# Kernel tuning notes

Hardware: AMD Instinct MI355X
Metric: run time of the kernel (lower is better)

The kernel has to match this reference:

```python
import jax, jax.numpy as jnp
import numpy as np

MAX_SHIFT = 20
DAILY_CYCLE = 288
HORIZON_OFFSET = 1


def _valid_shifts(T):
    shifts = sorted(set(list(range(-MAX_SHIFT, 1)) + [-(DAILY_CYCLE - HORIZON_OFFSET)]))
    return [s for s in shifts if 0 < abs(s) < T]


def setup_inputs() -> dict:
    key = jax.random.key(0)
    k1, k2 = jax.random.split(key)
    x = jax.random.normal(k1, (2, 320, 207, 64), dtype=jnp.float32)
    w = jax.random.normal(k2, (1, 1), dtype=jnp.float32)  # LearnableSimilarity linear weight
    return {"x": x, "w": w}


def reference(x, w):
    B, T, L, D = x.shape
    shifts = _valid_shifts(T)
    S = len(shifts)  # 21 for T=320

    # Build zero-padded shifted copies: for s<0, shifted[:, t] = x[:, t+|s|] (zeros at tail).
    sh_list = []
    for s in shifts:
        p = abs(s)
        pad = jnp.zeros((B, p, L, D), dtype=x.dtype)
        if s < 0:
            sh_list.append(jnp.concatenate([x[:, p:], pad], axis=1))
        else:
            sh_list.append(jnp.concatenate([pad, x[:, :-p]], axis=1))
    xs = jnp.stack(sh_list, axis=1)  # [B, S, T, L, D]

    # Learnable similarity = (x . y) * w; mean over T fused into the einsum.
    wscalar = w[0, 0]
    sim_avg = jnp.einsum('btld,bstmd->bslm', x, xs) * (wscalar / T)  # [B,S,L,L]  l=target, m=shifted

    # Faithful to original: softmax over joint (S*target-L) axis, then raw reshape to (L, S*L).
    flat = sim_avg.reshape(B, S * L, L)
    soft = jax.nn.softmax(flat, axis=1)
    attn = soft.reshape(B, L, S * L)  # NOTE: reshape, not transpose (matches torch .view)

    x_flat = xs.transpose(0, 2, 1, 3, 4).reshape(B, T, S * L, D)  # m index = s*L + link
    out = jnp.einsum('btmd,blm->btld', x_flat, attn)  # [B,T,L,D]
    return out
```

## Files before the change

kernel.cpp:

```cpp
#include <hip/hip_runtime.h>
#include <hip/hip_bf16.h>

#define B_DIM 2
#define T_DIM 320
#define L_DIM 207
#define D_DIM 64
#define S_DIM 21
#define J_TOT (S_DIM * L_DIM)
#define MPAD 224
#define IPAD 256
#define NSPLIT 4
#define TSPLIT 80
#define NCH_A 32
#define CH_A 136
#define NCH_P 128
#define CH_P 34
#define LD_ROW (L_DIM * D_DIM)

typedef __attribute__((ext_vector_type(8))) short bf16x8;
typedef __attribute__((ext_vector_type(4))) float f32x4;

__device__ inline unsigned short f2bf(float f) {
    unsigned int u = __builtin_bit_cast(unsigned int, f);
    u = (u + 0x7FFFu + ((u >> 16) & 1u)) >> 16;
    return (unsigned short)u;
}

__device__ inline int shift_p(int s) { return (s == 0) ? 287 : (21 - s); }
__device__ inline int imin(int a, int b) { return a < b ? a : b; }
__device__ inline int imax(int a, int b) { return a > b ? a : b; }

__device__ __forceinline__ void glds16(const void* g, void* l) {
    __builtin_amdgcn_global_load_lds(
        (const __attribute__((address_space(1))) void*)g,
        (__attribute__((address_space(3))) void*)l,
        16, 0, 0);
}

__global__ void __launch_bounds__(256) k_prep(const float* __restrict__ x,
                                              unsigned short* __restrict__ xbf,
                                              unsigned short* __restrict__ xt) {
    __shared__ float tile[L_DIM * 66];
    int bt = blockIdx.x;
    const float* src = x + (size_t)bt * LD_ROW;
    int tid = threadIdx.x;
    for (int idx = tid; idx < L_DIM * D_DIM; idx += 256) {
        int l = idx >> 6, d = idx & 63;
        tile[l * 66 + d] = src[idx];
    }
    __syncthreads();
    unsigned short* dst1 = xbf + (size_t)bt * LD_ROW;
    for (int idx = tid; idx < L_DIM * D_DIM; idx += 256) {
        int l = idx >> 6, d = idx & 63;
        dst1[idx] = f2bf(tile[l * 66 + d]);
    }
    unsigned short* dst2 = xt + (size_t)bt * (7 * 64 * 32);
    if (tid < MPAD) {
        int mc = tid >> 5, mi = tid & 31;
        for (int d = 0; d < D_DIM; ++d) {
            float v = (tid < L_DIM) ? tile[tid * 66 + d] : 0.0f;
            dst2[(mc * 64 + d) * 32 + mi] = f2bf(v);
        }
    }
}

__global__ void __launch_bounds__(256) k_sim(const unsigned short* __restrict__ xbf,
                                             float* __restrict__ part) {
    __shared__ __align__(16) unsigned short S[2][2][8192];

    int id = blockIdx.x;
    int bsplit = id & 7;
    int b = bsplit >> 2, split = bsplit & 3;
    int rest = id >> 3;
    int s = rest >> 2;
    int tile = rest & 3;
    int l0 = (tile >> 1) * 128, m0 = (tile & 1) * 128;

    int p = shift_p(s);
    int nt = T_DIM - p;
    int t0 = (split * nt) >> 2;
    int t1 = (((split + 1) * nt) >> 2);

    int tid = threadIdx.x;
    int wave = tid >> 6, lane = tid & 63;
    int wl = wave >> 1, wm = wave & 1;
    int fr = lane & 15, kg = lane >> 4;
    int x7 = fr & 7;

    int rN = 0, cN = 0;
#pragma unroll
    for (int g = 0; g < 4; ++g) {
        if (l0 + (g * 2 + wl) * 16 < L_DIM) rN = g + 1;
        if (m0 + (g * 2 + wm) * 16 < L_DIM) cN = g + 1;
    }

    int srcoff[4];
#pragma unroll
    for (int i = 0; i < 4; ++i) {
        int n = i * 256 + wave * 64 + lane;
        int row = n >> 3, c = n & 7;
        srcoff[i] = row * 128 + ((c ^ (row & 7)) * 16);
    }
    int wbase = wave * 1024;

    int cb0 = (kg ^ x7) * 16, cb1 = ((4 + kg) ^ x7) * 16;
    int aro[4], bro[4];
#pragma unroll
    for (int g = 0; g < 4; ++g) {
        aro[g] = ((g * 2 + wl) * 16 + fr) * 128;
        bro[g] = ((g * 2 + wm) * 16 + fr) * 128;
    }

    f32x4 acc[4][4];
#pragma unroll
    for (int i = 0; i < 4; ++i)
#pragma unroll
        for (int j = 0; j < 4; ++j) acc[i][j] = f32x4{0.f, 0.f, 0.f, 0.f};

    const size_t LDB = (size_t)LD_ROW * 2;
    const char* abase = (const char*)xbf + ((size_t)b * T_DIM * LD_ROW + (size_t)l0 * 64) * 2;
    const char* bbase = (const char*)xbf + ((size_t)(b * T_DIM + p) * LD_ROW + (size_t)m0 * 64) * 2;

    if (t1 > t0) {
        {
            const char* a = abase + (size_t)t0 * LDB;
            const char* bb = bbase + (size_t)t0 * LDB;
            char* lA = (char*)&S[0][0][0] + wbase;
            char* lB = (char*)&S[0][1][0] + wbase;
#pragma unroll
            for (int i = 0; i < 4; ++i) {
                glds16(a + srcoff[i], lA + i * 4096);
                glds16(bb + srcoff[i], lB + i * 4096);
            }
        }
        int cur = 0;
        for (int t = t0; t < t1; ++t) {
            bool more = (t + 1 < t1);
            if (more) {
                const char* a = abase + (size_t)(t + 1) * LDB;
                const char* bb = bbase + (size_t)(t + 1) * LDB;
                char* lA = (char*)&S[cur ^ 1][0][0] + wbase;
                char* lB = (char*)&S[cur ^ 1][1][0] + wbase;
#pragma unroll
                for (int i = 0; i < 4; ++i) {
                    glds16(a + srcoff[i], lA + i * 4096);
                    glds16(bb + srcoff[i], lB + i * 4096);
                }
                asm volatile("s_waitcnt vmcnt(8)" ::: "memory");
            } else {
                asm volatile("s_waitcnt vmcnt(0)" ::: "memory");
            }
            __builtin_amdgcn_s_barrier();
            asm volatile("" ::: "memory");
            const char* lA = (const char*)&S[cur][0][0];
            const char* lB = (const char*)&S[cur][1][0];
#pragma unroll
            for (int kd = 0; kd < 2; ++kd) {
                int cb = kd ? cb1 : cb0;
                bf16x8 af[4], bv[4];
#pragma unroll
                for (int g = 0; g < 4; ++g)
                    if (g < rN) af[g] = *(const bf16x8*)(lA + aro[g] + cb);
#pragma unroll
                for (int g = 0; g < 4; ++g)
                    if (g < cN) bv[g] = *(const bf16x8*)(lB + bro[g] + cb);
#pragma unroll
                for (int rg = 0; rg < 4; ++rg)
                    if (rg < rN)
#pragma unroll
                        for (int cg = 0; cg < 4; ++cg)
                            if (cg < cN)
                                acc[rg][cg] = __builtin_amdgcn_mfma_f32_16x16x32_bf16(
                                    af[rg], bv[cg], acc[rg][cg], 0, 0, 0);
            }
            asm volatile("" ::: "memory");
            __builtin_amdgcn_s_barrier();
            cur ^= 1;
        }
    }

    float* pdst = part + ((size_t)(split * B_DIM + b) * J_TOT + (size_t)s * L_DIM) * L_DIM;
#pragma unroll
    for (int rg = 0; rg < 4; ++rg)
#pragma unroll
        for (int cg = 0; cg < 4; ++cg) {
            int col = m0 + (cg * 2 + wm) * 16 + fr;
            if (col < L_DIM) {
#pragma unroll
                for (int r = 0; r < 4; ++r) {
                    int row = l0 + (rg * 2 + wl) * 16 + kg * 4 + r;
                    if (row < L_DIM) pdst[(size_t)row * L_DIM + col] = acc[rg][cg][r];
                }
            }
        }
}

__global__ void __launch_bounds__(256) k_sumexp(const float* __restrict__ part,
                                                const float* __restrict__ w,
                                                float* __restrict__ psum) {
    int c = blockIdx.x, b = blockIdx.y;
    int m = threadIdx.x;
    if (m >= L_DIM) return;
    float scale = w[0] / (float)T_DIM;
    int j0 = c * CH_A, j1 = imin(j0 + CH_A, J_TOT);
    float acc = 0.0f;
    for (int j = j0; j < j1; ++j) {
        float v = 0.0f;
#pragma unroll
        for (int r = 0; r < NSPLIT; ++r)
            v += part[((size_t)(r * B_DIM + b) * J_TOT + j) * L_DIM + m];
        acc += __expf(v * scale);
    }
    psum[(b * NCH_A + c) * L_DIM + m] = acc;
}

__global__ void __launch_bounds__(256) k_pack(const float* __restrict__ part,
                                              const float* __restrict__ w,
                                              const float* __restrict__ psum,
                                              unsigned short* __restrict__ pp) {
    __shared__ float sinv[L_DIM];
    int c = blockIdx.x, b = blockIdx.y;
    int tid = threadIdx.x;
    if (tid < L_DIM) {
        float g = 0.0f;
        for (int q = 0; q < NCH_A; ++q) g += psum[(b * NCH_A + q) * L_DIM + tid];
        sinv[tid] = 1.0f / g;
    }
    __syncthreads();
    if (tid >= MPAD) return;
    float scale = w[0] / (float)T_DIM;
    float inv = (tid < L_DIM) ? sinv[tid] : 0.0f;
    int mc = tid >> 5, mi = tid & 31;
    int j0 = c * CH_P, j1 = imin(j0 + CH_P, J_TOT);
    for (int j = j0; j < j1; ++j) {
        float pr = 0.0f;
        if (tid < L_DIM) {
            float v = 0.0f;
#pragma unroll
            for (int r = 0; r < NSPLIT; ++r)
                v += part[((size_t)(r * B_DIM + b) * J_TOT + j) * L_DIM + tid];
            pr = __expf(v * scale) * inv;
        }
        int i = j / S_DIM, s = j % S_DIM;
        pp[((((size_t)b * S_DIM + s) * 7 + mc) * IPAD + i) * 32 + mi] = f2bf(pr);
    }
}

__global__ void __launch_bounds__(256) k_out(const unsigned short* __restrict__ ppn,
                                             const unsigned short* __restrict__ xtn,
                                             float* __restrict__ out) {
    __shared__ __align__(16) unsigned short As[2][128 * 32];
    __shared__ __align__(16) unsigned short Bs[2][2][64 * 32];

    int id = blockIdx.x;
    int low = id & 7;
    int b = low >> 2, tr = low & 3;
    int rest = id >> 3;
    int tg = rest >> 1;
    int ih = rest & 1;
    int t0 = tr * TSPLIT + tg * 2;
    int i0 = ih * 128;

    int tid = threadIdx.x;
    int wave = tid >> 6, lane = tid & 63;
    int wt = wave >> 1, wi = wave & 1;
    int fr = lane & 15, kg = lane >> 4;
    int t = t0 + wt;

    const char* ppb = (const char*)ppn + (size_t)b * (S_DIM * 7 * IPAD * 32) * 2;
    const char* xtb = (const char*)xtn + (size_t)b * (T_DIM * 7 * 64 * 32) * 2;

    int asrc[2], bsrc[2];
#pragma unroll
    for (int i = 0; i < 2; ++i) {
        int n = wave * 128 + i * 64 + lane;
        int row = n >> 2, c = n & 3;
        asrc[i] = row * 64 + ((c ^ ((row >> 1) & 3)) * 16);
        int n2 = (wave & 1) * 128 + i * 64 + lane;
        int row2 = n2 >> 2, c2 = n2 & 3;
        bsrc[i] = row2 * 64 + ((c2 ^ ((row2 >> 1) & 3)) * 16);
    }
    int btau = wave >> 1;

    int cb = (kg ^ ((fr >> 1) & 3)) * 16;
    int aro[4], bro[4];
#pragma unroll
    for (int g = 0; g < 4; ++g) {
        aro[g] = (wi * 64 + g * 16 + fr) * 64;
        bro[g] = (g * 16 + fr) * 64;
    }

    f32x4 acc[4][4];
#pragma unroll
    for (int i = 0; i < 4; ++i)
#pragma unroll
        for (int j = 0; j < 4; ++j) acc[i][j] = f32x4{0.f, 0.f, 0.f, 0.f};

    int has0 = (t0 <= 32) ? 1 : 0;
    int sBegin = imax(1, t0 - 298);
    int ns = (21 - sBegin) + has0;

    auto sOf = [&](int k) { return (has0 && k == 0) ? 0 : sBegin + (k - has0); };

    auto stage = [&](int ss, int mc, int buf) {
        const char* ga = ppb + (((size_t)(ss * 7 + mc) * IPAD + i0) * 32) * 2;
        char* lA = (char*)&As[buf][0] + wave * 2048;
        glds16(ga + asrc[0], lA);
        glds16(ga + asrc[1], lA + 1024);
        int pp_ = shift_p(ss);
        int tau = imin(t0 + btau + pp_, T_DIM - 1);
        const char* gb = xtb + ((size_t)tau * 7 + mc) * 4096;
        char* lB = (char*)&Bs[buf][btau][0] + (wave & 1) * 2048;
        glds16(gb + bsrc[0], lB);
        glds16(gb + bsrc[1], lB + 1024);
    };

    stage(sOf(0), 0, 0);
    int cur = 0;
    for (int k = 0; k < ns; ++k) {
        int s = sOf(k);
        int p = shift_p(s);
        bool valid = (t + p < T_DIM);
        for (int mc = 0; mc < 7; ++mc) {
            bool more = (mc < 6) || (k + 1 < ns);
            if (more) {
                int s2 = (mc < 6) ? s : sOf(k + 1);
                int mc2 = (mc < 6) ? mc + 1 : 0;
                stage(s2, mc2, cur ^ 1);
                asm volatile("s_waitcnt vmcnt(4)" ::: "memory");
            } else {
                asm volatile("s_waitcnt vmcnt(0)" ::: "memory");
            }
            __builtin_amdgcn_s_barrier();
            asm volatile("" ::: "memory");
            if (valid) {
                const char* lA = (const char*)&As[cur][0];
                const char* lB = (const char*)&Bs[cur][wt][0];
                bf16x8 af[4], bv[4];
#pragma unroll
                for (int g = 0; g < 4; ++g) af[g] = *(const bf16x8*)(lA + aro[g] + cb);
#pragma unroll
                for (int g = 0; g < 4; ++g) bv[g] = *(const bf16x8*)(lB + bro[g] + cb);
#pragma unroll
                for (int rg = 0; rg < 4; ++rg)
#pragma unroll
                    for (int cg = 0; cg < 4; ++cg)
                        acc[rg][cg] = __builtin_amdgcn_mfma_f32_16x16x32_bf16(
                            af[rg], bv[cg], acc[rg][cg], 0, 0, 0);
            }
            asm volatile("" ::: "memory");
            __builtin_amdgcn_s_barrier();
            cur ^= 1;
        }
    }

    float* obase = out + (size_t)(b * T_DIM + t) * LD_ROW;
#pragma unroll
    for (int rg = 0; rg < 4; ++rg)
#pragma unroll
        for (int cg = 0; cg < 4; ++cg) {
            int d = cg * 16 + fr;
#pragma unroll
            for (int r = 0; r < 4; ++r) {
                int i = i0 + wi * 64 + rg * 16 + kg * 4 + r;
                if (i < L_DIM) obase[(size_t)i * D_DIM + d] = acc[rg][cg][r];
            }
        }
}

extern "C" void kernel_launch(void* const* d_in, const int* in_sizes, int n_in,
                              void* d_out, int out_size, void* d_ws, size_t ws_size,
                              hipStream_t stream) {
    const float* x = (const float*)d_in[0];
    const float* w = (const float*)d_in[1];
    float* out = (float*)d_out;

    char* ws = (char*)d_ws;
    size_t off = 0;
    auto carve = [&](size_t bytes) {
        void* p = ws + off;
        off += (bytes + 255) & ~(size_t)255;
        return p;
    };
    unsigned short* xbf = (unsigned short*)carve((size_t)B_DIM * T_DIM * LD_ROW * 2);
    unsigned short* xt  = (unsigned short*)carve((size_t)B_DIM * T_DIM * 7 * 64 * 32 * 2);
    float* part         = (float*)carve((size_t)NSPLIT * B_DIM * J_TOT * L_DIM * 4);
    float* psum         = (float*)carve((size_t)B_DIM * NCH_A * L_DIM * 4);
    size_t pp_bytes = (size_t)B_DIM * S_DIM * 7 * IPAD * 32 * 2;
    unsigned short* pp  = (unsigned short*)carve(pp_bytes);

    k_prep<<<B_DIM * T_DIM, 256, 0, stream>>>(x, xbf, xt);
    k_sim<<<8 * 84, 256, 0, stream>>>(xbf, part);
    k_sumexp<<<dim3(NCH_A, B_DIM), 256, 0, stream>>>(part, w, psum);
    hipMemsetAsync(pp, 0, pp_bytes, stream);
    k_pack<<<dim3(NCH_P, B_DIM), 256, 0, stream>>>(part, w, psum, pp);
    k_out<<<640, 256, 0, stream>>>(pp, xt, out);
}
```

Before: 391.8 us.

## Restructure similarity kernel to share x tiles across the 20 contiguous shifts

Replaces the per-shift similarity kernel with one that loops over time once per (l,m) tile and reuses each loaded x slab for all 20 consecutive shifts. It keeps a rolling 24-slot LDS window of B tiles and a register ring of fragments. The aim is to cut redundant global loads and launch work, since the old kernel re-read the same data once per shift. The large 287 shift stays in a separate small kernel, and a zero page stands in for out-of-range time steps. The cost is more register pressure, a more complex barrier and pipeline scheme, and one extra launch and memset.

Result: faster. 349.0 us (-10.9%).

```diff
diff --git a/kernel.cpp b/kernel.cpp
--- a/kernel.cpp
+++ b/kernel.cpp
@@ -16,6 +16,7 @@
 #define NCH_P 128
 #define CH_P 34
 #define LD_ROW (L_DIM * D_DIM)
+#define SLAB_B 26496
 
 typedef __attribute__((ext_vector_type(8))) short bf16x8;
 typedef __attribute__((ext_vector_type(4))) float f32x4;
@@ -64,19 +65,135 @@
     }
 }
 
-__global__ void __launch_bounds__(256) k_sim(const unsigned short* __restrict__ xbf,
-                                             float* __restrict__ part) {
+__global__ void __launch_bounds__(512, 2) k_simr(const unsigned short* __restrict__ xbf,
+                                                 const unsigned short* __restrict__ zpage,
+                                                 float* __restrict__ part) {
+    __shared__ __align__(16) unsigned short Asl[4][2048];
+    __shared__ __align__(16) unsigned short Bsl[24][2048];
+
+    int id = blockIdx.x;
+    int split = id / 98;
+    int r2 = id % 98;
+    int b = r2 & 1;
+    int pb = r2 >> 1;
+    int lfb = pb / 7, mfb = pb % 7;
+
+    int t0 = split * TSPLIT;
+    int t1 = t0 + TSPLIT;
+
+    int tid = threadIdx.x;
+    int w = tid >> 6, lane = tid & 63;
+    int wl = w & 1, wm = (w >> 1) & 1, h = w >> 2;
+    int fr = lane & 15, kg = lane >> 4;
+    int x7 = fr & 7;
+
+    int lf = lfb * 2 + wl;
+    int mf = mfb * 2 + wm;
+    bool wvalid = (lf <= 12) && (mf <= 12);
+
+    bool isA = (w < 4);
+    int gq = (w & 3) * 64 + lane;
+    int grow = gq >> 3, gc = gq & 7;
+    int srcoff = grow * 128 + ((gc ^ (grow & 7)) * 16);
+    int dstoff = (w & 3) * 1024;
+
+    const char* xb = (const char*)xbf;
+    size_t abase = (size_t)b * T_DIM * SLAB_B + lfb * 4096;
+    size_t bbase = (size_t)b * T_DIM * SLAB_B + mfb * 4096;
+
+    int lrA = wl * 16 + fr, lrB = wm * 16 + fr;
+    int c0 = ((0 + kg) ^ x7) * 16, c1 = ((4 + kg) ^ x7) * 16;
+    int aoff0 = lrA * 128 + c0, aoff1 = lrA * 128 + c1;
+    int boff0 = lrB * 128 + c0, boff1 = lrB * 128 + c1;
+
+    f32x4 acc[10];
+#pragma unroll
+    for (int j = 0; j < 10; ++j) acc[j] = f32x4{0.f, 0.f, 0.f, 0.f};
+    bf16x8 ring[10][2];
+
+    if (isA) {
+        glds16(xb + abase + (size_t)t0 * SLAB_B + srcoff, (char*)Asl[t0 & 3] + dstoff);
+    } else {
+        for (int k = 1; k <= 20; ++k) {
+            int tau = t0 + k;
+            const char* src = (tau < T_DIM) ? (xb + bbase + (size_t)tau * SLAB_B) : (const char*)zpage;
+            glds16(src + srcoff, (char*)Bsl[tau % 24] + dstoff);
+        }
+    }
+    asm volatile("s_waitcnt vmcnt(0)" ::: "memory");
+    __builtin_amdgcn_s_barrier();
+    asm volatile("" ::: "memory");
+    if (wvalid) {
+#pragma unroll
+        for (int j = 1; j <= 9; ++j) {
+            int tau = t0 + 20 - 10 * h - j;
+            const char* sb = (const char*)Bsl[tau % 24];
+            ring[10 - j][0] = *(const bf16x8*)(sb + boff0);
+            ring[10 - j][1] = *(const bf16x8*)(sb + boff1);
+        }
+    }
+
+    for (int tb = t0; tb < t1; tb += 10) {
+#pragma unroll
+        for (int u = 0; u < 10; ++u) {
+            int t = tb + u;
+            if (isA) {
+                int tn = t + 1;
+                const char* src = (tn < T_DIM) ? (xb + abase + (size_t)tn * SLAB_B) : (const char*)zpage;
+                glds16(src + srcoff, (char*)Asl[tn & 3] + dstoff);
+            } else {
+                int tau = t + 21;
+                const char* src = (tau < T_DIM) ? (xb + bbase + (size_t)tau * SLAB_B) : (const char*)zpage;
+                glds16(src + srcoff, (char*)Bsl[tau % 24] + dstoff);
+            }
+            asm volatile("s_waitcnt vmcnt(1)" ::: "memory");
+            __builtin_amdgcn_s_barrier();
+            asm volatile("" ::: "memory");
+            if (wvalid) {
+                const char* sa = (const char*)Asl[t & 3];
+                bf16x8 a0 = *(const bf16x8*)(sa + aoff0);
+                bf16x8 a1 = *(const bf16x8*)(sa + aoff1);
+                int tauf = t + 20 - 10 * h;
+                const char* sb = (const char*)Bsl[tauf % 24];
+                ring[u][0] = *(const bf16x8*)(sb + boff0);
+                ring[u][1] = *(const bf16x8*)(sb + boff1);
+#pragma unroll
+                for (int j = 0; j < 10; ++j) {
+                    acc[j] = __builtin_amdgcn_mfma_f32_16x16x32_bf16(a0, ring[(u - j + 10) % 10][0], acc[j], 0, 0, 0);
+                    acc[j] = __builtin_amdgcn_mfma_f32_16x16x32_bf16(a1, ring[(u - j + 10) % 10][1], acc[j], 0, 0, 0);
+                }
+            }
+        }
+    }
+
+    int col = mf * 16 + fr;
+    if (col < L_DIM) {
+        float* pbase = part + (size_t)(split * B_DIM + b) * J_TOT * L_DIM;
+#pragma unroll
+        for (int j = 0; j < 10; ++j) {
+            int s = 10 * h + 1 + j;
+#pragma unroll
+            for (int r = 0; r < 4; ++r) {
+                int row = lf * 16 + kg * 4 + r;
+                if (row < L_DIM)
+                    pbase[((size_t)s * L_DIM + row) * L_DIM + col] = acc[j][r];
+            }
+        }
+    }
+}
+
+__global__ void __launch_bounds__(256) k_sim0(const unsigned short* __restrict__ xbf,
+                                              float* __restrict__ part) {
     __shared__ __align__(16) unsigned short S[2][2][8192];
 
     int id = blockIdx.x;
-    int bsplit = id & 7;
-    int b = bsplit >> 2, split = bsplit & 3;
-    int rest = id >> 3;
-    int s = rest >> 2;
-    int tile = rest & 3;
+    int tile = id & 3;
+    int rest = id >> 2;
+    int split = rest & 3;
+    int b = rest >> 2;
     int l0 = (tile >> 1) * 128, m0 = (tile & 1) * 128;
 
-    int p = shift_p(s);
+    const int p = 287;
     int nt = T_DIM - p;
     int t0 = (split * nt) >> 2;
     int t1 = (((split + 1) * nt) >> 2);
@@ -179,7 +296,7 @@
         }
     }
 
-    float* pdst = part + ((size_t)(split * B_DIM + b) * J_TOT + (size_t)s * L_DIM) * L_DIM;
+    float* pdst = part + ((size_t)(split * B_DIM + b) * J_TOT + (size_t)0 * L_DIM) * L_DIM;
 #pragma unroll
     for (int rg = 0; rg < 4; ++rg)
 #pragma unroll
@@ -388,9 +505,12 @@
     float* psum         = (float*)carve((size_t)B_DIM * NCH_A * L_DIM * 4);
     size_t pp_bytes = (size_t)B_DIM * S_DIM * 7 * IPAD * 32 * 2;
     unsigned short* pp  = (unsigned short*)carve(pp_bytes);
+    unsigned short* zpage = (unsigned short*)carve(4096);
 
     k_prep<<<B_DIM * T_DIM, 256, 0, stream>>>(x, xbf, xt);
-    k_sim<<<8 * 84, 256, 0, stream>>>(xbf, part);
+    hipMemsetAsync(zpage, 0, 4096, stream);
+    k_simr<<<NSPLIT * 98, 512, 0, stream>>>(xbf, zpage, part);
+    k_sim0<<<B_DIM * NSPLIT * 4, 256, 0, stream>>>(xbf, part);
     k_sumexp<<<dim3(NCH_A, B_DIM), 256, 0, stream>>>(part, w, psum);
     hipMemsetAsync(pp, 0, pp_bytes, stream);
     k_pack<<<dim3(NCH_P, B_DIM), 256, 0, stream>>>(part, w, psum, pp);
```
